# Kernel tuning notes

Measured on AMD Instinct MI355X. Metric: run time of the kernel, lower is better.

## Reference

```python
import jax, jax.numpy as jnp
import numpy as np

E, C, H, W = 512, 64, 28, 28
N_CORNERS = 256


def setup_inputs() -> dict:
    key = jax.random.key(0)
    k1, k2, k3 = jax.random.split(key, 3)
    x = jax.random.normal(k1, (E, C, H, W), dtype=jnp.float32)
    # aggregator: Conv2d(4*C, 64, kernel_size=1, bias=False) -> weight [64, 4*C]
    W_agg = jax.random.normal(k2, (64, 4 * C), dtype=jnp.float32) * (1.0 / np.sqrt(4 * C))
    # each edge connects two corners
    edge_corner = jax.random.randint(k3, (E, 2), 0, N_CORNERS, dtype=jnp.int64)
    eids = jnp.arange(E, dtype=jnp.int64)
    # rows of [corner_idx, edge_idx], two per edge (consistent with edge_corner)
    corner_edge_pairs = jnp.concatenate([
        jnp.stack([edge_corner[:, 0], eids], axis=-1),
        jnp.stack([edge_corner[:, 1], eids], axis=-1),
    ], axis=0)
    return {"x": x, "W_agg": W_agg, "corner_edge_pairs": corner_edge_pairs,
            "edge_corner": edge_corner, "num_corners": N_CORNERS}


def reference(x, W_agg, corner_edge_pairs, edge_corner, num_corners):
    # scatter-mean edge features onto corners (index_add_ + count/clamp)
    seg = corner_edge_pairs[:, 0]
    gathered = x[corner_edge_pairs[:, 1]]                      # [2E, C, H, W]
    corner_features = jax.ops.segment_sum(gathered, seg, num_segments=num_corners)
    count = jax.ops.segment_sum(jnp.ones((corner_edge_pairs.shape[0],), x.dtype),
                                seg, num_segments=num_corners)
    corner_features = corner_features / jnp.clip(count, 1.0)[:, None, None, None]
    # gather back per edge endpoints
    left_x = corner_features[edge_corner[:, 0]]                # [E, C, H, W]
    right_x = corner_features[edge_corner[:, 1]]               # [E, C, H, W]
    global_x = jnp.max(x, axis=0, keepdims=True)               # [1, C, H, W]
    cat = jnp.concatenate([x, left_x, right_x,
                           jnp.broadcast_to(global_x, x.shape)], axis=1)  # [E,4C,H,W]
    # 1x1 conv, no bias, + ReLU
    out = jnp.einsum('echw,oc->eohw', cat, W_agg)
    return jax.nn.relu(out)
```

## Files before the change

kernel.cpp:

```cpp
#include <hip/hip_runtime.h>
#include <hip/hip_bf16.h>
#include <cstdint>

#define E_N   512
#define C_N   64
#define HW_N  784
#define CHW_N 50176
#define CHW4  12544
#define NC    256

typedef __attribute__((ext_vector_type(8))) short bf16x8;
typedef __attribute__((ext_vector_type(4))) float f32x4;
typedef __attribute__((ext_vector_type(8))) unsigned short us8;

__device__ __forceinline__ unsigned short bf16_rne(float f, float& hif) {
    unsigned int u = __float_as_uint(f);
    unsigned int r = u + 0x7FFFu + ((u >> 16) & 1u);
    unsigned short h = (unsigned short)(r >> 16);
    hif = __uint_as_float((unsigned int)h << 16);
    return h;
}

__device__ __forceinline__ void cvt8(const float* f, bf16x8& hi, bf16x8& lo) {
    unsigned int hw_[4], lw_[4];
    #pragma unroll
    for (int p = 0; p < 4; ++p) {
        float a = f[2 * p], b = f[2 * p + 1];
        unsigned int hp;
        asm("v_cvt_pk_bf16_f32 %0, %1, %2" : "=v"(hp) : "v"(a), "v"(b));
        float ha = __uint_as_float(hp << 16);
        float hb = __uint_as_float(hp & 0xFFFF0000u);
        float la = a - ha, lb = b - hb;
        unsigned int lp;
        asm("v_cvt_pk_bf16_f32 %0, %1, %2" : "=v"(lp) : "v"(la), "v"(lb));
        hw_[p] = hp; lw_[p] = lp;
    }
    union { unsigned int u[4]; bf16x8 v; } cu, cl;
    #pragma unroll
    for (int p = 0; p < 4; ++p) { cu.u[p] = hw_[p]; cl.u[p] = lw_[p]; }
    hi = cu.v; lo = cl.v;
}

__global__ void prep_k(const int* __restrict__ ec, const float* __restrict__ W,
                       int* __restrict__ adj_start, int* __restrict__ adj_edge,
                       float* __restrict__ inv_count,
                       unsigned short* __restrict__ Whi, unsigned short* __restrict__ Wlo)
{
    __shared__ int cnt[NC];
    __shared__ int st[NC + 1];
    int tid = threadIdx.x;
    if (tid < NC) cnt[tid] = 0;
    __syncthreads();
    for (int e = tid; e < E_N; e += 256) {
        atomicAdd(&cnt[ec[2 * e] & (NC - 1)], 1);
        atomicAdd(&cnt[ec[2 * e + 1] & (NC - 1)], 1);
    }
    __syncthreads();
    if (tid == 0) {
        int s = 0;
        for (int c = 0; c < NC; ++c) { st[c] = s; s += cnt[c]; }
        st[NC] = s;
    }
    __syncthreads();
    if (tid < NC) {
        adj_start[tid] = st[tid];
        inv_count[tid] = 1.0f / (float)((cnt[tid] > 1) ? cnt[tid] : 1);
        cnt[tid] = st[tid];
    }
    if (tid == 0) adj_start[NC] = st[NC];
    __syncthreads();
    for (int e = tid; e < E_N; e += 256) {
        adj_edge[atomicAdd(&cnt[ec[2 * e] & (NC - 1)], 1)] = e;
        adj_edge[atomicAdd(&cnt[ec[2 * e + 1] & (NC - 1)], 1)] = e;
    }
    for (int i = tid; i < 64 * 192; i += 256) {
        int o = i / 192, k = i - o * 192;
        float w = W[o * 256 + k];
        float hif;
        unsigned short hi = bf16_rne(w, hif);
        float d;
        unsigned short lo = bf16_rne(w - hif, d);
        Whi[i] = hi;
        Wlo[i] = lo;
    }
}

__global__ void gmax_part_k(const float* __restrict__ x, float* __restrict__ part)
{
    int p4 = blockIdx.x * 256 + threadIdx.x;
    const float4* p = reinterpret_cast<const float4*>(x) + (size_t)(blockIdx.y * 64) * CHW4 + p4;
    float4 m = make_float4(-INFINITY, -INFINITY, -INFINITY, -INFINITY);
    #pragma unroll 4
    for (int i = 0; i < 64; ++i) {
        float4 v = p[(size_t)i * CHW4];
        m.x = fmaxf(m.x, v.x); m.y = fmaxf(m.y, v.y);
        m.z = fmaxf(m.z, v.z); m.w = fmaxf(m.w, v.w);
    }
    reinterpret_cast<float4*>(part)[blockIdx.y * CHW4 + p4] = m;
}

__global__ void gmax_reduce_k(const float* __restrict__ part, float* __restrict__ gmax)
{
    int p4 = blockIdx.x * 256 + threadIdx.x;
    const float4* p = reinterpret_cast<const float4*>(part);
    float4 m = p[p4];
    #pragma unroll
    for (int i = 1; i < 8; ++i) {
        float4 v = p[i * CHW4 + p4];
        m.x = fmaxf(m.x, v.x); m.y = fmaxf(m.y, v.y);
        m.z = fmaxf(m.z, v.z); m.w = fmaxf(m.w, v.w);
    }
    reinterpret_cast<float4*>(gmax)[p4] = m;
}

__global__ void g4_k(const float* __restrict__ W, const float* __restrict__ gmax,
                     float* __restrict__ g4)
{
    int j4 = blockIdx.x * 256 + threadIdx.x;
    int o  = (j4 * 4) / HW_N;
    int hw = j4 * 4 - o * HW_N;
    float4 acc = make_float4(0.f, 0.f, 0.f, 0.f);
    #pragma unroll 8
    for (int c = 0; c < 64; ++c) {
        float w = W[o * 256 + 192 + c];
        float4 g = *reinterpret_cast<const float4*>(gmax + c * HW_N + hw);
        acc.x += w * g.x; acc.y += w * g.y; acc.z += w * g.z; acc.w += w * g.w;
    }
    *reinterpret_cast<float4*>(g4 + (size_t)j4 * 4) = acc;
}

__global__ void cf_k(const float* __restrict__ x, const int* __restrict__ adj_start,
                     const int* __restrict__ adj_edge, const float* __restrict__ inv_count,
                     float* __restrict__ cf)
{
    int c  = blockIdx.y;
    int p4 = blockIdx.x * 256 + threadIdx.x;
    float4 acc = make_float4(0.f, 0.f, 0.f, 0.f);
    int s0 = adj_start[c], s1 = adj_start[c + 1];
    for (int i = s0; i < s1; ++i) {
        int e = adj_edge[i];
        float4 v = *reinterpret_cast<const float4*>(x + (size_t)e * CHW_N + (size_t)p4 * 4);
        acc.x += v.x; acc.y += v.y; acc.z += v.z; acc.w += v.w;
    }
    float ic = inv_count[c];
    acc.x *= ic; acc.y *= ic; acc.z *= ic; acc.w *= ic;
    *reinterpret_cast<float4*>(cf + (size_t)c * CHW_N + (size_t)p4 * 4) = acc;
}

__global__ __launch_bounds__(256) void fused_mfma_k(
    const float* __restrict__ x, const float* __restrict__ cf,
    const unsigned short* __restrict__ Whi, const unsigned short* __restrict__ Wlo,
    const float* __restrict__ g4, const int* __restrict__ ec,
    float* __restrict__ out)
{
    __shared__ unsigned short Ah[64][200], Al[64][200];
    __shared__ const float* sb[3][8];
    __shared__ int eArr[8], hwArr[8];

    int tid = threadIdx.x;
    int jbase = blockIdx.x * 128;

    if (tid < 8) {
        int j16 = jbase + tid * 16;
        int e   = j16 / HW_N;
        int hw0 = j16 - e * HW_N;
        eArr[tid]  = e;
        hwArr[tid] = hw0;
        int c0 = ec[2 * e]     & (NC - 1);
        int c1 = ec[2 * e + 1] & (NC - 1);
        sb[0][tid] = x  + (size_t)e  * CHW_N + hw0;
        sb[1][tid] = cf + (size_t)c0 * CHW_N + hw0;
        sb[2][tid] = cf + (size_t)c1 * CHW_N + hw0;
    }

    #pragma unroll
    for (int i = 0; i < 6; ++i) {
        int chunk = tid + i * 256;
        int row = chunk / 24, c8 = chunk % 24;
        *reinterpret_cast<us8*>(&Ah[row][c8 * 8]) =
            *reinterpret_cast<const us8*>(Whi + row * 192 + c8 * 8);
        *reinterpret_cast<us8*>(&Al[row][c8 * 8]) =
            *reinterpret_cast<const us8*>(Wlo + row * 192 + c8 * 8);
    }
    __syncthreads();

    int lane = tid & 63;
    int wv   = tid >> 6;
    int r16  = lane & 15;
    int q    = lane >> 4;

    f32x4 acc[4][2];
    #pragma unroll
    for (int a = 0; a < 4; ++a)
        #pragma unroll
        for (int b = 0; b < 2; ++b) acc[a][b] = (f32x4){0.f, 0.f, 0.f, 0.f};

    const float* pB[3][2];
    #pragma unroll
    for (int seg = 0; seg < 3; ++seg)
        #pragma unroll
        for (int jt = 0; jt < 2; ++jt)
            pB[seg][jt] = sb[seg][wv * 2 + jt] + q * 8 * HW_N + r16;

    #pragma unroll
    for (int s = 0; s < 6; ++s) {
        const int seg = s >> 1;
        const int kr0 = (s & 1) * 32;
        const int k0  = s * 32;

        float f0[8], f1[8];
        #pragma unroll
        for (int i = 0; i < 8; ++i) f0[i] = pB[seg][0][(kr0 + i) * HW_N];
        #pragma unroll
        for (int i = 0; i < 8; ++i) f1[i] = pB[seg][1][(kr0 + i) * HW_N];

        bf16x8 ah[4], al[4];
        #pragma unroll
        for (int ot = 0; ot < 4; ++ot) {
            ah[ot] = *reinterpret_cast<const bf16x8*>(&Ah[ot * 16 + r16][k0 + q * 8]);
            al[ot] = *reinterpret_cast<const bf16x8*>(&Al[ot * 16 + r16][k0 + q * 8]);
        }

        bf16x8 bh[2], bl[2];
        cvt8(f0, bh[0], bl[0]);
        cvt8(f1, bh[1], bl[1]);

        #pragma unroll
        for (int ot = 0; ot < 4; ++ot)
            #pragma unroll
            for (int jt = 0; jt < 2; ++jt) {
                acc[ot][jt] = __builtin_amdgcn_mfma_f32_16x16x32_bf16(ah[ot], bh[jt], acc[ot][jt], 0, 0, 0);
                acc[ot][jt] = __builtin_amdgcn_mfma_f32_16x16x32_bf16(ah[ot], bl[jt], acc[ot][jt], 0, 0, 0);
                acc[ot][jt] = __builtin_amdgcn_mfma_f32_16x16x32_bf16(al[ot], bh[jt], acc[ot][jt], 0, 0, 0);
            }
    }

    int orb = q << 2;
    #pragma unroll
    for (int ot = 0; ot < 4; ++ot)
        #pragma unroll
        for (int jt = 0; jt < 2; ++jt) {
            int g  = wv * 2 + jt;
            int e  = eArr[g];
            int hw = hwArr[g] + r16;
            #pragma unroll
            for (int r = 0; r < 4; ++r) {
                int o = ot * 16 + orb + r;
                float v = acc[ot][jt][r] + g4[o * HW_N + hw];
                out[(size_t)e * CHW_N + o * HW_N + hw] = fmaxf(v, 0.f);
            }
        }
}

extern "C" void kernel_launch(void* const* d_in, const int* in_sizes, int n_in,
                              void* d_out, int out_size, void* d_ws, size_t ws_size,
                              hipStream_t stream)
{
    const float* x  = (const float*)d_in[0];
    const float* W  = (const float*)d_in[1];
    const int*   ec = (const int*)d_in[3];
    float* out      = (float*)d_out;

    float* ws_f      = (float*)d_ws;
    float* cf        = ws_f;
    float* part      = cf + (size_t)NC * CHW_N;
    float* gmax      = part + 8 * CHW_N;
    float* g4        = gmax + CHW_N;
    unsigned short* Whi = (unsigned short*)(g4 + CHW_N);
    unsigned short* Wlo = Whi + 12288;
    int*   adj_start = (int*)(Wlo + 12288);
    int*   adj_edge  = adj_start + 272;
    float* inv_count = (float*)(adj_edge + 1024);

    prep_k<<<1, 256, 0, stream>>>(ec, W, adj_start, adj_edge, inv_count, Whi, Wlo);
    gmax_part_k<<<dim3(49, 8), 256, 0, stream>>>(x, part);
    gmax_reduce_k<<<49, 256, 0, stream>>>(part, gmax);
    g4_k<<<49, 256, 0, stream>>>(W, gmax, g4);
    cf_k<<<dim3(49, NC), 256, 0, stream>>>(x, adj_start, adj_edge, inv_count, cf);
    fused_mfma_k<<<3136, 256, 0, stream>>>(x, cf, Whi, Wlo, g4, ec, out);
}
```

Baseline: 303.2 us.

## Fuse gmax reduce with g4, prefetch B tiles, drop Al LDS staging

Several changes at once. The gmax reduction and the global-max weight projection are merged into one kernel that keeps the max in shared memory, and the serial prefix sum in prep becomes a wave shuffle scan. In the main MFMA kernel, each wave computes its own edge pointers instead of staging them through shared memory, and B operand loads are double-buffered one k-step ahead. The low-half weights are now read directly from global memory rather than LDS, which halves shared memory per block and targets 4 blocks per SM via launch bounds, at the risk of extra global or cache traffic for Al.

```diff
diff --git a/kernel.cpp b/kernel.cpp
--- a/kernel.cpp
+++ b/kernel.cpp
@@ -8,6 +8,7 @@
 #define CHW_N 50176
 #define CHW4  12544
 #define NC    256
+#define GHW   28
 
 typedef __attribute__((ext_vector_type(8))) short bf16x8;
 typedef __attribute__((ext_vector_type(4))) float f32x4;
@@ -56,10 +57,19 @@
         atomicAdd(&cnt[ec[2 * e + 1] & (NC - 1)], 1);
     }
     __syncthreads();
-    if (tid == 0) {
-        int s = 0;
-        for (int c = 0; c < NC; ++c) { st[c] = s; s += cnt[c]; }
-        st[NC] = s;
+    if (tid < 64) {
+        int b = tid * 4;
+        int v0 = cnt[b], v1 = cnt[b + 1], v2 = cnt[b + 2], v3 = cnt[b + 3];
+        int s4 = v0 + v1 + v2 + v3;
+        int incl = s4;
+        #pragma unroll
+        for (int off = 1; off < 64; off <<= 1) {
+            int t = __shfl_up(incl, off);
+            if (tid >= off) incl += t;
+        }
+        int ex = incl - s4;
+        st[b] = ex; st[b + 1] = ex + v0; st[b + 2] = ex + v0 + v1; st[b + 3] = ex + v0 + v1 + v2;
+        if (tid == 63) st[NC] = incl;
     }
     __syncthreads();
     if (tid < NC) {
@@ -99,34 +109,33 @@
     reinterpret_cast<float4*>(part)[blockIdx.y * CHW4 + p4] = m;
 }
 
-__global__ void gmax_reduce_k(const float* __restrict__ part, float* __restrict__ gmax)
-{
-    int p4 = blockIdx.x * 256 + threadIdx.x;
-    const float4* p = reinterpret_cast<const float4*>(part);
-    float4 m = p[p4];
-    #pragma unroll
-    for (int i = 1; i < 8; ++i) {
-        float4 v = p[i * CHW4 + p4];
-        m.x = fmaxf(m.x, v.x); m.y = fmaxf(m.y, v.y);
-        m.z = fmaxf(m.z, v.z); m.w = fmaxf(m.w, v.w);
-    }
-    reinterpret_cast<float4*>(gmax)[p4] = m;
-}
-
-__global__ void g4_k(const float* __restrict__ W, const float* __restrict__ gmax,
-                     float* __restrict__ g4)
-{
-    int j4 = blockIdx.x * 256 + threadIdx.x;
-    int o  = (j4 * 4) / HW_N;
-    int hw = j4 * 4 - o * HW_N;
-    float4 acc = make_float4(0.f, 0.f, 0.f, 0.f);
-    #pragma unroll 8
-    for (int c = 0; c < 64; ++c) {
-        float w = W[o * 256 + 192 + c];
-        float4 g = *reinterpret_cast<const float4*>(gmax + c * HW_N + hw);
-        acc.x += w * g.x; acc.y += w * g.y; acc.z += w * g.z; acc.w += w * g.w;
-    }
-    *reinterpret_cast<float4*>(g4 + (size_t)j4 * 4) = acc;
+__global__ void g4r_k(const float* __restrict__ part, const float* __restrict__ W,
+                      float* __restrict__ g4)
+{
+    __shared__ float gm[64][GHW];
+    int tid = threadIdx.x;
+    int hw0 = blockIdx.x * GHW;
+    #pragma unroll
+    for (int k = 0; k < 7; ++k) {
+        int idx = tid + k * 256;
+        int c = idx / GHW, hw = idx - c * GHW;
+        float m = -INFINITY;
+        #pragma unroll
+        for (int i = 0; i < 8; ++i)
+            m = fmaxf(m, part[(size_t)i * CHW_N + c * HW_N + hw0 + hw]);
+        gm[c][hw] = m;
+    }
+    __syncthreads();
+    #pragma unroll
+    for (int k = 0; k < 7; ++k) {
+        int idx = tid + k * 256;
+        int o = idx / GHW, hw = idx - o * GHW;
+        float acc = 0.f;
+        #pragma unroll 8
+        for (int c = 0; c < 64; ++c)
+            acc += W[o * 256 + 192 + c] * gm[c][hw];
+        g4[o * HW_N + hw0 + hw] = acc;
+    }
 }
 
 __global__ void cf_k(const float* __restrict__ x, const int* __restrict__ adj_start,
@@ -147,31 +156,44 @@
     *reinterpret_cast<float4*>(cf + (size_t)c * CHW_N + (size_t)p4 * 4) = acc;
 }
 
-__global__ __launch_bounds__(256) void fused_mfma_k(
+__global__ __launch_bounds__(256, 4) void fused_mfma_k(
     const float* __restrict__ x, const float* __restrict__ cf,
     const unsigned short* __restrict__ Whi, const unsigned short* __restrict__ Wlo,
     const float* __restrict__ g4, const int* __restrict__ ec,
     float* __restrict__ out)
 {
-    __shared__ unsigned short Ah[64][200], Al[64][200];
-    __shared__ const float* sb[3][8];
-    __shared__ int eArr[8], hwArr[8];
-
-    int tid = threadIdx.x;
+    __shared__ unsigned short Ah[64][200];
+
+    int tid  = threadIdx.x;
+    int lane = tid & 63;
+    int wv   = tid >> 6;
+    int r16  = lane & 15;
+    int q    = lane >> 4;
     int jbase = blockIdx.x * 128;
 
-    if (tid < 8) {
-        int j16 = jbase + tid * 16;
-        int e   = j16 / HW_N;
-        int hw0 = j16 - e * HW_N;
-        eArr[tid]  = e;
-        hwArr[tid] = hw0;
-        int c0 = ec[2 * e]     & (NC - 1);
-        int c1 = ec[2 * e + 1] & (NC - 1);
-        sb[0][tid] = x  + (size_t)e  * CHW_N + hw0;
-        sb[1][tid] = cf + (size_t)c0 * CHW_N + hw0;
-        sb[2][tid] = cf + (size_t)c1 * CHW_N + hw0;
-    }
+    int j16a = jbase + (wv * 2) * 16;
+    int ea   = j16a / HW_N;
+    int hwa  = j16a - ea * HW_N;
+    int j16b = j16a + 16;
+    int eb   = j16b / HW_N;
+    int hwb  = j16b - eb * HW_N;
+    int c0a = ec[2 * ea] & (NC - 1), c1a = ec[2 * ea + 1] & (NC - 1);
+    int c0b = ec[2 * eb] & (NC - 1), c1b = ec[2 * eb + 1] & (NC - 1);
+
+    const float* pB0[3];
+    const float* pB1[3];
+    pB0[0] = x  + (size_t)ea  * CHW_N + hwa + q * 8 * HW_N + r16;
+    pB1[0] = x  + (size_t)eb  * CHW_N + hwb + q * 8 * HW_N + r16;
+    pB0[1] = cf + (size_t)c0a * CHW_N + hwa + q * 8 * HW_N + r16;
+    pB1[1] = cf + (size_t)c0b * CHW_N + hwb + q * 8 * HW_N + r16;
+    pB0[2] = cf + (size_t)c1a * CHW_N + hwa + q * 8 * HW_N + r16;
+    pB1[2] = cf + (size_t)c1b * CHW_N + hwb + q * 8 * HW_N + r16;
+
+    float fa[8], fb[8], ga[8], gb[8];
+    #pragma unroll
+    for (int i = 0; i < 8; ++i) fa[i] = pB0[0][i * HW_N];
+    #pragma unroll
+    for (int i = 0; i < 8; ++i) fb[i] = pB1[0][i * HW_N];
 
     #pragma unroll
     for (int i = 0; i < 6; ++i) {
@@ -179,15 +201,10 @@
         int row = chunk / 24, c8 = chunk % 24;
         *reinterpret_cast<us8*>(&Ah[row][c8 * 8]) =
             *reinterpret_cast<const us8*>(Whi + row * 192 + c8 * 8);
-        *reinterpret_cast<us8*>(&Al[row][c8 * 8]) =
-            *reinterpret_cast<const us8*>(Wlo + row * 192 + c8 * 8);
-    }
-    __syncthreads();
-
-    int lane = tid & 63;
-    int wv   = tid >> 6;
-    int r16  = lane & 15;
-    int q    = lane >> 4;
+    }
+    __syncthreads();
+
+    const unsigned short* pAl = Wlo + r16 * 192 + q * 8;
 
     f32x4 acc[4][2];
     #pragma unroll
@@ -195,35 +212,31 @@
         #pragma unroll
         for (int b = 0; b < 2; ++b) acc[a][b] = (f32x4){0.f, 0.f, 0.f, 0.f};
 
-    const float* pB[3][2];
-    #pragma unroll
-    for (int seg = 0; seg < 3; ++seg)
-        #pragma unroll
-        for (int jt = 0; jt < 2; ++jt)
-            pB[seg][jt] = sb[seg][wv * 2 + jt] + q * 8 * HW_N + r16;
-
     #pragma unroll
     for (int s = 0; s < 6; ++s) {
-        const int seg = s >> 1;
-        const int kr0 = (s & 1) * 32;
-        const int k0  = s * 32;
-
-        float f0[8], f1[8];
-        #pragma unroll
-        for (int i = 0; i < 8; ++i) f0[i] = pB[seg][0][(kr0 + i) * HW_N];
-        #pragma unroll
-        for (int i = 0; i < 8; ++i) f1[i] = pB[seg][1][(kr0 + i) * HW_N];
+        const int k0 = s * 32;
+        float* c0 = (s & 1) ? ga : fa;
+        float* c1 = (s & 1) ? gb : fb;
+        float* n0 = (s & 1) ? fa : ga;
+        float* n1 = (s & 1) ? fb : gb;
+        if (s < 5) {
+            const int nseg = (s + 1) >> 1, nkr = ((s + 1) & 1) * 32;
+            #pragma unroll
+            for (int i = 0; i < 8; ++i) n0[i] = pB0[nseg][(nkr + i) * HW_N];
+            #pragma unroll
+            for (int i = 0; i < 8; ++i) n1[i] = pB1[nseg][(nkr + i) * HW_N];
+        }
 
         bf16x8 ah[4], al[4];
         #pragma unroll
         for (int ot = 0; ot < 4; ++ot) {
             ah[ot] = *reinterpret_cast<const bf16x8*>(&Ah[ot * 16 + r16][k0 + q * 8]);
-            al[ot] = *reinterpret_cast<const bf16x8*>(&Al[ot * 16 + r16][k0 + q * 8]);
+            al[ot] = *reinterpret_cast<const bf16x8*>(pAl + (ot * 16) * 192 + k0);
         }
 
         bf16x8 bh[2], bl[2];
-        cvt8(f0, bh[0], bl[0]);
-        cvt8(f1, bh[1], bl[1]);
+        cvt8(c0, bh[0], bl[0]);
+        cvt8(c1, bh[1], bl[1]);
 
         #pragma unroll
         for (int ot = 0; ot < 4; ++ot)
@@ -240,9 +253,8 @@
     for (int ot = 0; ot < 4; ++ot)
         #pragma unroll
         for (int jt = 0; jt < 2; ++jt) {
-            int g  = wv * 2 + jt;
-            int e  = eArr[g];
-            int hw = hwArr[g] + r16;
+            int e  = jt ? eb : ea;
+            int hw = (jt ? hwb : hwa) + r16;
             #pragma unroll
             for (int r = 0; r < 4; ++r) {
                 int o = ot * 16 + orb + r;
@@ -264,8 +276,7 @@
     float* ws_f      = (float*)d_ws;
     float* cf        = ws_f;
     float* part      = cf + (size_t)NC * CHW_N;
-    float* gmax      = part + 8 * CHW_N;
-    float* g4        = gmax + CHW_N;
+    float* g4        = part + 8 * CHW_N;
     unsigned short* Whi = (unsigned short*)(g4 + CHW_N);
     unsigned short* Wlo = Whi + 12288;
     int*   adj_start = (int*)(Wlo + 12288);
@@ -274,8 +285,7 @@
 
     prep_k<<<1, 256, 0, stream>>>(ec, W, adj_start, adj_edge, inv_count, Whi, Wlo);
     gmax_part_k<<<dim3(49, 8), 256, 0, stream>>>(x, part);
-    gmax_reduce_k<<<49, 256, 0, stream>>>(part, gmax);
-    g4_k<<<49, 256, 0, stream>>>(W, gmax, g4);
+    g4r_k<<<28, 256, 0, stream>>>(part, W, g4);
     cf_k<<<dim3(49, NC), 256, 0, stream>>>(x, adj_start, adj_edge, inv_count, cf);
     fused_mfma_k<<<3136, 256, 0, stream>>>(x, cf, Whi, Wlo, g4, ec, out);
 }
```

Result: slower. 314.1 us (+3.6%).
